# Kernel tuning notes

Hardware: AMD Instinct MI355X
Metric: run time of the kernel (lower is better)

The kernel has to match this reference:

```python
import jax, jax.numpy as jnp
import numpy as np

SEQ_LEN = 16384
IN_DIM = 2048
STATE_DIM = 2048


def setup_inputs() -> dict:
    key = jax.random.key(0)
    k_xs, k_lam, k_win, k_c, k_d = jax.random.split(key, 5)
    xs = jax.random.normal(k_xs, (SEQ_LEN, IN_DIM), dtype=jnp.float32)
    # diagonal state-transition values in (0, 1) for stability
    lam = jax.random.uniform(k_lam, (STATE_DIM,), dtype=jnp.float32)
    w_in = jax.random.normal(k_win, (STATE_DIM, IN_DIM), dtype=jnp.float32) / np.float32(np.sqrt(IN_DIM))
    c_out = jax.random.normal(k_c, (IN_DIM, STATE_DIM), dtype=jnp.float32) / np.float32(np.sqrt(STATE_DIM))
    d_skip = jax.random.normal(k_d, (IN_DIM,), dtype=jnp.float32)
    return {"xs": xs, "lam": lam, "w_in": w_in, "c_out": c_out, "d_skip": d_skip}


def _ssm_cell(a, b):
    # Faithful replication of BaseSSMLayer.ssm_cell (including its use of
    # matrix_pow_i * matrix_pow_i for the first component, exactly as in source).
    matrix_pow_i, bx_i = a
    matrix_pow_j, bx_j = b
    return (matrix_pow_i * matrix_pow_i, matrix_pow_j * bx_i + bx_j)


def reference(xs, lam, w_in, c_out, d_skip):
    seq_len = xs.shape[0]
    # discretize: broadcast diagonal lambda over the sequence -> [L, N]
    lambda_elements = jnp.broadcast_to(lam, (seq_len, lam.shape[0]))
    # preprocess_inputs: vmap(w_in @ x) == xs @ w_in.T  -> [L, N]
    w_in_xs = jnp.einsum('li,ni->ln', xs, w_in)
    _, hs = jax.lax.associative_scan(_ssm_cell, (lambda_elements, w_in_xs))
    # postprocess: y_t = C h_t + D * x_t  -> [L, in_dim]
    return jnp.einsum('ln,on->lo', hs, c_out) + xs * d_skip
```

## Files before the change

### kernel.cpp

```cpp
#include <hip/hip_runtime.h>

#define SEQ   16384
#define DIM   2048
#define CHUNK 128
#define NCHUNK (SEQ / CHUNK)

typedef __attribute__((ext_vector_type(8))) short  short8;
typedef __attribute__((ext_vector_type(4))) short  short4v;
typedef __attribute__((ext_vector_type(4))) float  floatx4;

static __device__ __forceinline__ float bf2f(short s) {
    return __uint_as_float(((unsigned)(unsigned short)s) << 16);
}
static __device__ __forceinline__ short f2bf(float f) {
    unsigned u = __float_as_uint(f);
    u += 0x7fff + ((u >> 16) & 1);
    return (short)(u >> 16);
}

__global__ void cast_kernel(const float* __restrict__ in, short* __restrict__ out, int n4) {
    int i = blockIdx.x * blockDim.x + threadIdx.x;
    if (i >= n4) return;
    float4 v = ((const float4*)in)[i];
    short4v s;
    s.x = f2bf(v.x); s.y = f2bf(v.y); s.z = f2bf(v.z); s.w = f2bf(v.w);
    ((short4v*)out)[i] = s;
}


#define BAR   __builtin_amdgcn_s_barrier()
#define PRIO1 __builtin_amdgcn_s_setprio(1)
#define PRIO0 __builtin_amdgcn_s_setprio(0)
#define LGKM0 asm volatile("s_waitcnt lgkmcnt(0)" ::: "memory")
#define VMC4  asm volatile("s_waitcnt vmcnt(4)" ::: "memory")
#define VMC0  asm volatile("s_waitcnt vmcnt(0)" ::: "memory")

#define STAGE_A(b, h, t) do { \
    const short* _s = Abase + (size_t)(h) * 128 * K + (size_t)(t) * 64; \
    __builtin_amdgcn_global_load_lds(_s + gOff0, &As[b][h][c0 * 8], 16, 0, 0); \
    __builtin_amdgcn_global_load_lds(_s + gOff1, &As[b][h][c1 * 8], 16, 0, 0); \
} while (0)
#define STAGE_B(b, h, t) do { \
    const short* _s = Bbase + (size_t)(h) * 128 * K + (size_t)(t) * 64; \
    __builtin_amdgcn_global_load_lds(_s + gOff0, &Bs[b][h][c0 * 8], 16, 0, 0); \
    __builtin_amdgcn_global_load_lds(_s + gOff1, &Bs[b][h][c1 * 8], 16, 0, 0); \
} while (0)

#define LDA_(dst, b, mh) \
    _Pragma("unroll") \
    for (int mi = 0; mi < 4; mi++) { \
        _Pragma("unroll") \
        for (int ks = 0; ks < 2; ks++) \
            dst[mi][ks] = *(const short8*)&As[b][mh][(arow + mi * 16) * 64 + \
                                                     ((((ks << 2) | quad) ^ sx) << 3)]; \
    }
#define LDB_(dst, b, nh) \
    _Pragma("unroll") \
    for (int ni = 0; ni < 2; ni++) { \
        _Pragma("unroll") \
        for (int ks = 0; ks < 2; ks++) \
            dst[ni][ks] = *(const short8*)&Bs[b][nh][(brow + ni * 16) * 64 + \
                                                     ((((ks << 2) | quad) ^ sx) << 3)]; \
    }
#define MMA(mh, nh, Aset, Bset) \
    _Pragma("unroll") \
    for (int mi = 0; mi < 4; mi++) { \
        _Pragma("unroll") \
        for (int ni = 0; ni < 2; ni++) { \
            acc[mh][nh][mi][ni] = __builtin_amdgcn_mfma_f32_16x16x32_bf16( \
                Aset[mi][0], Bset[ni][0], acc[mh][nh][mi][ni], 0, 0, 0); \
            acc[mh][nh][mi][ni] = __builtin_amdgcn_mfma_f32_16x16x32_bf16( \
                Aset[mi][1], Bset[ni][1], acc[mh][nh][mi][ni], 0, 0, 0); \
        } \
    }

template<int FUSE>
__global__ __launch_bounds__(512, 2)
void gemm_bt(const short* __restrict__ A, const short* __restrict__ B,
             short* __restrict__ Cbf, float* __restrict__ Cf,
             const float* __restrict__ xs, const float* __restrict__ dskip)
{
    constexpr int K  = DIM;
    constexpr int NT = K / 64;

    __shared__ alignas(16) short As[2][2][128 * 64];
    __shared__ alignas(16) short Bs[2][2][128 * 64];

    const int tid = threadIdx.x;
    const int raw  = blockIdx.y * gridDim.x + blockIdx.x;
    const int xcd  = raw & 7;
    const int slot = raw >> 3;
    const int m0   = ((xcd << 3) | (slot >> 3)) * 256;
    const int n0   = (slot & 7) * 256;

    const int lane = tid & 63;
    const int wv   = tid >> 6;
    const int wrow = wv >> 2;
    const int wcol = wv & 3;
    const int l16  = lane & 15;
    const int quad = lane >> 4;
    const int sx   = l16 & 7;
    const int arow = wrow * 64 + l16;
    const int brow = wcol * 32 + l16;

    const int c0 = tid, c1 = tid + 512;
    const int r0 = c0 >> 3, r1 = c1 >> 3;
    const size_t gOff0 = (size_t)r0 * K + (size_t)((((c0 & 7) ^ (r0 & 7))) * 8);
    const size_t gOff1 = (size_t)r1 * K + (size_t)((((c1 & 7) ^ (r1 & 7))) * 8);
    const short* Abase = A + (size_t)m0 * K;
    const short* Bbase = B + (size_t)n0 * K;

    short8  A0[4][2], A1[4][2], B0[2][2], B1[2][2];
    floatx4 acc[2][2][4][2] = {};

    STAGE_A(0, 0, 0); STAGE_B(0, 0, 0); STAGE_A(0, 1, 0); STAGE_B(0, 1, 0);
    STAGE_A(1, 0, 1); STAGE_B(1, 0, 1);
    VMC4;
    BAR;
    LDA_(A0, 0, 0); LDB_(B0, 0, 0);
    STAGE_A(1, 1, 1); STAGE_B(1, 1, 1);

    for (int i = 0; i < NT / 2; ++i) {
        const int tE = (2 * i + 2) & (NT - 1);
        const int tO = (2 * i + 3) & (NT - 1);

        LGKM0;
        STAGE_A(0, 0, tE);
        LDB_(B1, 0, 1); LDA_(A1, 0, 1);
        PRIO1; MMA(0, 0, A0, B0); PRIO0;
        BAR;
        STAGE_B(0, 0, tE);
        PRIO1; MMA(0, 1, A0, B1); PRIO0;
        BAR;
        LGKM0;
        VMC4;
        STAGE_A(0, 1, tE);
        PRIO1; MMA(1, 0, A1, B0); PRIO0;
        LDA_(A0, 1, 0); LDB_(B0, 1, 0);
        BAR;
        STAGE_B(0, 1, tE);
        PRIO1; MMA(1, 1, A1, B1); PRIO0;
        BAR;

        LGKM0;
        STAGE_A(1, 0, tO);
        LDB_(B1, 1, 1); LDA_(A1, 1, 1);
        PRIO1; MMA(0, 0, A0, B0); PRIO0;
        BAR;
        STAGE_B(1, 0, tO);
        PRIO1; MMA(0, 1, A0, B1); PRIO0;
        BAR;
        LGKM0;
        VMC4;
        STAGE_A(1, 1, tO);
        PRIO1; MMA(1, 0, A1, B0); PRIO0;
        LDA_(A0, 0, 0); LDB_(B0, 0, 0);
        BAR;
        STAGE_B(1, 1, tO);
        PRIO1; MMA(1, 1, A1, B1); PRIO0;
        BAR;
    }
    VMC0;

    if (FUSE == 0) {
        #pragma unroll
        for (int mh = 0; mh < 2; mh++)
        #pragma unroll
        for (int mi = 0; mi < 4; mi++) {
            const int rb = m0 + wrow * 64 + mh * 128 + mi * 16 + quad * 4;
            #pragma unroll
            for (int nh = 0; nh < 2; nh++)
            #pragma unroll
            for (int ni = 0; ni < 2; ni++) {
                const int cc = n0 + wcol * 32 + nh * 128 + ni * 16 + l16;
                #pragma unroll
                for (int r = 0; r < 4; r++)
                    Cbf[(size_t)(rb + r) * DIM + cc] = f2bf(acc[mh][nh][mi][ni][r]);
            }
        }
    } else {
        float dsk[2][2];
        #pragma unroll
        for (int nh = 0; nh < 2; nh++)
        #pragma unroll
        for (int ni = 0; ni < 2; ni++)
            dsk[nh][ni] = dskip[n0 + wcol * 32 + nh * 128 + ni * 16 + l16];
        #pragma unroll
        for (int mh = 0; mh < 2; mh++)
        #pragma unroll
        for (int mi = 0; mi < 4; mi++) {
            const int rb = m0 + wrow * 64 + mh * 128 + mi * 16 + quad * 4;
            #pragma unroll
            for (int nh = 0; nh < 2; nh++)
            #pragma unroll
            for (int ni = 0; ni < 2; ni++) {
                const int cc = n0 + wcol * 32 + nh * 128 + ni * 16 + l16;
                #pragma unroll
                for (int r = 0; r < 4; r++) {
                    size_t idx = (size_t)(rb + r) * DIM + cc;
                    Cf[idx] = acc[mh][nh][mi][ni][r] + xs[idx] * dsk[nh][ni];
                }
            }
        }
    }
}

__global__ void scan_pass1(const short* __restrict__ bx, const float* __restrict__ lam,
                           float* __restrict__ blockLast)
{
    int q     = blockIdx.x * 256 + threadIdx.x;
    int n     = q * 4;
    int chunk = blockIdx.y;
    float4 lm = *(const float4*)&lam[n];
    const uint2* p = (const uint2*)(bx + (size_t)chunk * CHUNK * DIM) + q;
    float h0 = 0.f, h1 = 0.f, h2 = 0.f, h3 = 0.f;
    #pragma unroll 16
    for (int i = 0; i < CHUNK; i++) {
        uint2 v = p[(size_t)i * (DIM / 4)];
        h0 = fmaf(lm.x, h0, bf2f((short)(v.x & 0xffffu)));
        h1 = fmaf(lm.y, h1, bf2f((short)(v.x >> 16)));
        h2 = fmaf(lm.z, h2, bf2f((short)(v.y & 0xffffu)));
        h3 = fmaf(lm.w, h3, bf2f((short)(v.y >> 16)));
    }
    float4 o; o.x = h0; o.y = h1; o.z = h2; o.w = h3;
    *(float4*)&blockLast[(size_t)chunk * DIM + n] = o;
}

__global__ void scan_pass2(float* __restrict__ blockLast, const float* __restrict__ lam)
{
    int n = blockIdx.x * 256 + threadIdx.x;
    float lm = lam[n];
    float p = lm;
    #pragma unroll
    for (int i = 0; i < 7; i++) p = p * p;
    float carry = 0.f;
    #pragma unroll 4
    for (int c = 0; c < NCHUNK; c++) {
        float t = blockLast[(size_t)c * DIM + n];
        blockLast[(size_t)c * DIM + n] = carry;
        carry = fmaf(p, carry, t);
    }
}

__global__ void scan_pass3(short* __restrict__ bxh, const float* __restrict__ lam,
                           const float* __restrict__ carry)
{
    int q     = blockIdx.x * 256 + threadIdx.x;
    int n     = q * 4;
    int chunk = blockIdx.y;
    float4 lm = *(const float4*)&lam[n];
    float4 cv = *(const float4*)&carry[(size_t)chunk * DIM + n];
    float h0 = cv.x, h1 = cv.y, h2 = cv.z, h3 = cv.w;
    uint2* p = (uint2*)(bxh + (size_t)chunk * CHUNK * DIM) + q;
    #pragma unroll 16
    for (int i = 0; i < CHUNK; i++) {
        uint2 v = p[(size_t)i * (DIM / 4)];
        h0 = fmaf(lm.x, h0, bf2f((short)(v.x & 0xffffu)));
        h1 = fmaf(lm.y, h1, bf2f((short)(v.x >> 16)));
        h2 = fmaf(lm.z, h2, bf2f((short)(v.y & 0xffffu)));
        h3 = fmaf(lm.w, h3, bf2f((short)(v.y >> 16)));
        uint2 o;
        o.x = (unsigned)(unsigned short)f2bf(h0) | ((unsigned)(unsigned short)f2bf(h1) << 16);
        o.y = (unsigned)(unsigned short)f2bf(h2) | ((unsigned)(unsigned short)f2bf(h3) << 16);
        p[(size_t)i * (DIM / 4)] = o;
    }
}

extern "C" void kernel_launch(void* const* d_in, const int* in_sizes, int n_in,
                              void* d_out, int out_size, void* d_ws, size_t ws_size,
                              hipStream_t stream)
{
    const float* xs    = (const float*)d_in[0];
    const float* lam   = (const float*)d_in[1];
    const float* w_in  = (const float*)d_in[2];
    const float* c_out = (const float*)d_in[3];
    const float* dskip = (const float*)d_in[4];
    float* out = (float*)d_out;

    char*  ws    = (char*)d_ws;
    short* bxh   = (short*)ws;
    short* w_bf  = (short*)(ws + (size_t)64 * 1024 * 1024);
    short* c_bf  = (short*)(ws + (size_t)72 * 1024 * 1024);
    short* xs_bf = (short*)d_out;
    float* blkl  = (float*)((char*)d_out + (size_t)100 * 1024 * 1024);

    cast_kernel<<<SEQ * DIM / 4 / 256, 256, 0, stream>>>(xs, xs_bf, SEQ * DIM / 4);
    cast_kernel<<<DIM * DIM / 4 / 256, 256, 0, stream>>>(w_in, w_bf, DIM * DIM / 4);
    cast_kernel<<<DIM * DIM / 4 / 256, 256, 0, stream>>>(c_out, c_bf, DIM * DIM / 4);

    dim3 ggrid(DIM / 256, SEQ / 256);
    gemm_bt<0><<<ggrid, 512, 0, stream>>>(xs_bf, w_bf, bxh, nullptr, nullptr, nullptr);

    dim3 sgrid(DIM / 1024, NCHUNK);
    scan_pass1<<<sgrid, 256, 0, stream>>>(bxh, lam, blkl);
    scan_pass2<<<DIM / 256, 256, 0, stream>>>(blkl, lam);
    scan_pass3<<<sgrid, 256, 0, stream>>>(bxh, lam, blkl);

    gemm_bt<1><<<ggrid, 512, 0, stream>>>(bxh, c_bf, nullptr, out, xs, dskip);
}
```

Before: 551.4 us.

## Restructure GEMM main-loop software pipeline and merge three cast launches into one

```diff
diff --git a/kernel.cpp b/kernel.cpp
--- a/kernel.cpp
+++ b/kernel.cpp
@@ -18,9 +18,17 @@
     return (short)(u >> 16);
 }
 
-__global__ void cast_kernel(const float* __restrict__ in, short* __restrict__ out, int n4) {
-    int i = blockIdx.x * blockDim.x + threadIdx.x;
-    if (i >= n4) return;
+#define NB_XS (SEQ * DIM / 4 / 256)
+#define NB_W  (DIM * DIM / 4 / 256)
+__global__ void cast3_kernel(const float* __restrict__ xs,   short* __restrict__ xs_o,
+                             const float* __restrict__ w,    short* __restrict__ w_o,
+                             const float* __restrict__ c,    short* __restrict__ c_o)
+{
+    int b = blockIdx.x;
+    const float* in; short* out; int i;
+    if (b < NB_XS)            { in = xs; out = xs_o; i = b * 256 + threadIdx.x; }
+    else if (b < NB_XS + NB_W){ in = w;  out = w_o;  i = (b - NB_XS) * 256 + threadIdx.x; }
+    else                      { in = c;  out = c_o;  i = (b - NB_XS - NB_W) * 256 + threadIdx.x; }
     float4 v = ((const float4*)in)[i];
     short4v s;
     s.x = f2bf(v.x); s.y = f2bf(v.y); s.z = f2bf(v.z); s.w = f2bf(v.w);
@@ -31,8 +39,8 @@
 #define BAR   __builtin_amdgcn_s_barrier()
 #define PRIO1 __builtin_amdgcn_s_setprio(1)
 #define PRIO0 __builtin_amdgcn_s_setprio(0)
-#define LGKM0 asm volatile("s_waitcnt lgkmcnt(0)" ::: "memory")
-#define VMC4  asm volatile("s_waitcnt vmcnt(4)" ::: "memory")
+#define VMC2  asm volatile("s_waitcnt vmcnt(2)" ::: "memory")
+#define VMC1  asm volatile("s_waitcnt vmcnt(1)" ::: "memory")
 #define VMC0  asm volatile("s_waitcnt vmcnt(0)" ::: "memory")
 
 #define STAGE_A(b, h, t) do { \
@@ -46,7 +54,7 @@
     __builtin_amdgcn_global_load_lds(_s + gOff1, &Bs[b][h][c1 * 8], 16, 0, 0); \
 } while (0)
 
-#define LDA_(dst, b, mh) \
+#define READ_A8(dst, b, mh) \
     _Pragma("unroll") \
     for (int mi = 0; mi < 4; mi++) { \
         _Pragma("unroll") \
@@ -54,7 +62,7 @@
             dst[mi][ks] = *(const short8*)&As[b][mh][(arow + mi * 16) * 64 + \
                                                      ((((ks << 2) | quad) ^ sx) << 3)]; \
     }
-#define LDB_(dst, b, nh) \
+#define READ_B4(dst, b, nh) \
     _Pragma("unroll") \
     for (int ni = 0; ni < 2; ni++) { \
         _Pragma("unroll") \
@@ -110,54 +118,56 @@
     const short* Abase = A + (size_t)m0 * K;
     const short* Bbase = B + (size_t)n0 * K;
 
-    short8  A0[4][2], A1[4][2], B0[2][2], B1[2][2];
+    short8  aE[4][2], aO[4][2], bE[2][2], bO[2][2];
     floatx4 acc[2][2][4][2] = {};
 
-    STAGE_A(0, 0, 0); STAGE_B(0, 0, 0); STAGE_A(0, 1, 0); STAGE_B(0, 1, 0);
-    STAGE_A(1, 0, 1); STAGE_B(1, 0, 1);
-    VMC4;
+    STAGE_A(0, 0, 0); STAGE_B(0, 0, 0); STAGE_B(0, 1, 0);
+    STAGE_A(0, 1, 0);
+    VMC1;
     BAR;
-    LDA_(A0, 0, 0); LDB_(B0, 0, 0);
-    STAGE_A(1, 1, 1); STAGE_B(1, 1, 1);
+    READ_A8(aE, 0, 0); READ_B4(bE, 0, 0);
 
     for (int i = 0; i < NT / 2; ++i) {
-        const int tE = (2 * i + 2) & (NT - 1);
-        const int tO = (2 * i + 3) & (NT - 1);
-
-        LGKM0;
-        STAGE_A(0, 0, tE);
-        LDB_(B1, 0, 1); LDA_(A1, 0, 1);
-        PRIO1; MMA(0, 0, A0, B0); PRIO0;
-        BAR;
-        STAGE_B(0, 0, tE);
-        PRIO1; MMA(0, 1, A0, B1); PRIO0;
-        BAR;
-        LGKM0;
-        VMC4;
-        STAGE_A(0, 1, tE);
-        PRIO1; MMA(1, 0, A1, B0); PRIO0;
-        LDA_(A0, 1, 0); LDB_(B0, 1, 0);
-        BAR;
-        STAGE_B(0, 1, tE);
-        PRIO1; MMA(1, 1, A1, B1); PRIO0;
-        BAR;
-
-        LGKM0;
-        STAGE_A(1, 0, tO);
-        LDB_(B1, 1, 1); LDA_(A1, 1, 1);
-        PRIO1; MMA(0, 0, A0, B0); PRIO0;
-        BAR;
-        STAGE_B(1, 0, tO);
-        PRIO1; MMA(0, 1, A0, B1); PRIO0;
-        BAR;
-        LGKM0;
-        VMC4;
-        STAGE_A(1, 1, tO);
-        PRIO1; MMA(1, 0, A1, B0); PRIO0;
-        LDA_(A0, 0, 0); LDB_(B0, 0, 0);
-        BAR;
-        STAGE_B(1, 1, tO);
-        PRIO1; MMA(1, 1, A1, B1); PRIO0;
+        const int t1 = 2 * i + 1;
+        const int t2 = (2 * i + 2) & (NT - 1);
+
+        READ_B4(bO, 0, 1);
+        STAGE_A(1, 0, t1); STAGE_B(1, 0, t1);
+        PRIO1; MMA(0, 0, aE, bE); PRIO0;
+        VMC2;
+        BAR;
+        READ_A8(aO, 0, 1);
+        STAGE_B(1, 1, t1); STAGE_A(1, 1, t1);
+        PRIO1; MMA(0, 1, aE, bO); PRIO0;
+        VMC2;
+        BAR;
+        PRIO1; MMA(1, 0, aO, bE); PRIO0;
+        READ_B4(bE, 1, 0);
+        BAR;
+        PRIO1; MMA(1, 1, aO, bO); PRIO0;
+        READ_A8(aE, 1, 0);
+        VMC1;
+        BAR;
+
+        READ_B4(bO, 1, 1);
+        STAGE_A(0, 0, t2); STAGE_B(0, 0, t2);
+        PRIO1; MMA(0, 0, aE, bE); PRIO0;
+        VMC2;
+        BAR;
+
+        READ_A8(aO, 1, 1);
+        STAGE_B(0, 1, t2); STAGE_A(0, 1, t2);
+        PRIO1; MMA(0, 1, aE, bO); PRIO0;
+        VMC2;
+        BAR;
+
+        PRIO1; MMA(1, 0, aO, bE); PRIO0;
+        READ_B4(bE, 0, 0);
+        BAR;
+
+        PRIO1; MMA(1, 1, aO, bO); PRIO0;
+        READ_A8(aE, 0, 0);
+        VMC1;
         BAR;
     }
     VMC0;
@@ -284,9 +294,7 @@
     short* xs_bf = (short*)d_out;
     float* blkl  = (float*)((char*)d_out + (size_t)100 * 1024 * 1024);
 
-    cast_kernel<<<SEQ * DIM / 4 / 256, 256, 0, stream>>>(xs, xs_bf, SEQ * DIM / 4);
-    cast_kernel<<<DIM * DIM / 4 / 256, 256, 0, stream>>>(w_in, w_bf, DIM * DIM / 4);
-    cast_kernel<<<DIM * DIM / 4 / 256, 256, 0, stream>>>(c_out, c_bf, DIM * DIM / 4);
+    cast3_kernel<<<NB_XS + 2 * NB_W, 256, 0, stream>>>(xs, xs_bf, w_in, w_bf, c_out, c_bf);
 
     dim3 ggrid(DIM / 256, SEQ / 256);
     gemm_bt<0><<<ggrid, 512, 0, stream>>>(xs_bf, w_bf, bxh, nullptr, nullptr, nullptr);
```

New measurement: 569.1 us. 3.2% more time.
